# Performance work log

Measured on AMD Instinct MI355X. Metric: run time of the kernel, lower is better.

## Reference

```python
import jax, jax.numpy as jnp
import numpy as np

S, I, H, FC, O = 16384, 64, 1024, 128, 1


def setup_inputs() -> dict:
    key = jax.random.key(0)
    ks = jax.random.split(key, 9)
    s_lstm = 1.0 / np.sqrt(H)
    return {
        "input_seq": jax.random.normal(ks[0], (S, I), jnp.float32),
        "W_ih": jax.random.uniform(ks[1], (4 * H, I), jnp.float32, -s_lstm, s_lstm),
        "W_hh": jax.random.uniform(ks[2], (4 * H, H), jnp.float32, -s_lstm, s_lstm),
        "b_ih": jax.random.uniform(ks[3], (4 * H,), jnp.float32, -s_lstm, s_lstm),
        "b_hh": jax.random.uniform(ks[4], (4 * H,), jnp.float32, -s_lstm, s_lstm),
        "fc1_w": jax.random.uniform(ks[5], (FC, H), jnp.float32, -s_lstm, s_lstm),
        "fc1_b": jax.random.uniform(ks[6], (FC,), jnp.float32, -s_lstm, s_lstm),
        "fc2_w": jax.random.uniform(ks[7], (O, FC), jnp.float32, -1.0 / np.sqrt(FC), 1.0 / np.sqrt(FC)),
        "fc2_b": jax.random.uniform(ks[8], (O,), jnp.float32, -1.0 / np.sqrt(FC), 1.0 / np.sqrt(FC)),
    }


def _lstm_scan(x, W_ih, W_hh, b_ih, b_hh):
    # PyTorch gate order: i, f, g, o. batch=1 collapsed; x: [S, I]
    xg = x @ W_ih.T + (b_ih + b_hh)  # precompute input-side gates: [S, 4H]

    def step(carry, xg_t):
        h, c = carry
        gates = xg_t + h @ W_hh.T
        i, f, g, o = jnp.split(gates, 4)
        i = jax.nn.sigmoid(i)
        f = jax.nn.sigmoid(f)
        g = jnp.tanh(g)
        o = jax.nn.sigmoid(o)
        c = f * c + i * g
        h = o * jnp.tanh(c)
        return (h, c), h

    h0 = jnp.zeros((H,), x.dtype)
    c0 = jnp.zeros((H,), x.dtype)
    _, hs = jax.lax.scan(step, (h0, c0), xg)
    return hs  # [S, H]


def reference(input_seq, W_ih, W_hh, b_ih, b_hh, fc1_w, fc1_b, fc2_w, fc2_b):
    hs = _lstm_scan(input_seq, W_ih, W_hh, b_ih, b_hh)       # [S, H]
    x = jax.nn.relu(hs)                                       # relu on LSTM outputs
    x = jax.nn.relu(x @ fc1_w.T + fc1_b)                      # [S, 128]
    x = x @ fc2_w.T + fc2_b                                   # [S, 1]
    return x[-1]                                              # [1]
```

## Files before the change

### kernel.cpp

```cpp
#include <hip/hip_runtime.h>
#include <hip/hip_fp16.h>


#define S_LEN 16384
#define I_DIM 64
#define H_DIM 1024
#define NBLK  64
#define NTHR  1024

__device__ __forceinline__ float sigmoidf_(float x) { return 1.0f / (1.0f + __expf(-x)); }
__device__ __forceinline__ float tanh_fast(float x) { return 1.0f - 2.0f / (__expf(2.0f * x) + 1.0f); }

__device__ __forceinline__ unsigned pack_pair(unsigned tag, float h) {
    return (tag << 16) | (unsigned)__half_as_ushort(__float2half(h));
}
__device__ __forceinline__ float unpack_val(unsigned pk) {
    return __half2float(__ushort_as_half((unsigned short)(pk & 0xFFFFu)));
}

__global__ __launch_bounds__(NTHR, 4) void lstm_persistent(
    const float* __restrict__ xseq,
    const float* __restrict__ W_ih,
    const float* __restrict__ W_hh,
    const float* __restrict__ b_ih,
    const float* __restrict__ b_hh,
    unsigned* __restrict__ pairs)
{
    const int b   = blockIdx.x;
    const int tid = threadIdx.x;
    const int w   = tid >> 6;
    const int c   = tid & 63;
    const int g   = w >> 2;
    const int r0  = (w & 3) * 4;

    __shared__ float4 h_stage[H_DIM / 4];
    __shared__ float  x_stage[2][I_DIM];
    __shared__ float  gs[64];
    __shared__ float  bias_s[64];

    float4 wh[4][4];
    float  wi[4];
    #pragma unroll
    for (int q = 0; q < 4; ++q) {
        const int grow = g * H_DIM + 16 * b + r0 + q;
        const float4* wr = (const float4*)(W_hh + (size_t)grow * H_DIM);
        #pragma unroll
        for (int s = 0; s < 4; ++s) wh[q][s] = wr[s * 64 + c];
        wi[q] = W_ih[(size_t)grow * I_DIM + c];
    }
    if (tid < 64) {
        const int grow = (tid >> 4) * H_DIM + 16 * b + (tid & 15);
        bias_s[tid] = b_ih[grow] + b_hh[grow];
    }
    float cst = 0.0f;
    if (tid < H_DIM / 4) h_stage[tid] = make_float4(0.f, 0.f, 0.f, 0.f);
    if (tid < 16) ((float4*)x_stage[0])[tid] = ((const float4*)xseq)[tid];
    const bool own = (tid >> 4) == b;
    __syncthreads();

    for (int t = 0; t < S_LEN; ++t) {
        if (tid < 16 && t + 1 < S_LEN)
            ((float4*)x_stage[(t + 1) & 1])[tid] =
                ((const float4*)(xseq + (size_t)(t + 1) * I_DIM))[tid];

        float acc[4] = {0.f, 0.f, 0.f, 0.f};
        #pragma unroll
        for (int s = 0; s < 4; ++s) {
            const float4 hv = h_stage[s * 64 + c];
            #pragma unroll
            for (int q = 0; q < 4; ++q) {
                acc[q] = fmaf(wh[q][s].x, hv.x, acc[q]);
                acc[q] = fmaf(wh[q][s].y, hv.y, acc[q]);
                acc[q] = fmaf(wh[q][s].z, hv.z, acc[q]);
                acc[q] = fmaf(wh[q][s].w, hv.w, acc[q]);
            }
        }
        {
            const float xv = x_stage[t & 1][c];
            #pragma unroll
            for (int q = 0; q < 4; ++q) acc[q] = fmaf(wi[q], xv, acc[q]);
        }
        #pragma unroll
        for (int q = 0; q < 4; ++q) {
            #pragma unroll
            for (int off = 32; off > 0; off >>= 1)
                acc[q] += __shfl_xor(acc[q], off, 64);
        }
        if (c == 0) {
            #pragma unroll
            for (int q = 0; q < 4; ++q) gs[g * 16 + r0 + q] = acc[q];
        }
        __syncthreads();

        if (tid < 16) {
            const float pi  = gs[tid]      + bias_s[tid];
            const float pfg = gs[16 + tid] + bias_s[16 + tid];
            const float pg  = gs[32 + tid] + bias_s[32 + tid];
            const float po  = gs[48 + tid] + bias_s[48 + tid];
            const float ig = sigmoidf_(pi);
            const float fg = sigmoidf_(pfg);
            const float gg = tanh_fast(pg);
            const float og = sigmoidf_(po);
            cst = fg * cst + ig * gg;
            const float h = og * tanh_fast(cst);
            const unsigned pk = pack_pair((unsigned)(t + 1), h);
            __hip_atomic_store(&pairs[(size_t)(t & 1) * H_DIM + 16 * b + tid], pk,
                               __ATOMIC_RELAXED, __HIP_MEMORY_SCOPE_AGENT);
            ((float*)h_stage)[16 * b + tid] = unpack_val(pk);
        }

        if (t == S_LEN - 1) break;

        if (!own) {
            const unsigned tag = (unsigned)(t + 1);
            const unsigned* p = &pairs[(size_t)(t & 1) * H_DIM + tid];
            unsigned pk;
            for (;;) {
                pk = __hip_atomic_load(p, __ATOMIC_RELAXED, __HIP_MEMORY_SCOPE_AGENT);
                if ((pk >> 16) == tag) break;
                __builtin_amdgcn_s_sleep(1);
            }
            ((float*)h_stage)[tid] = unpack_val(pk);
        }
        __syncthreads();
    }
}

__global__ __launch_bounds__(256) void fc_head(
    const unsigned* __restrict__ pairs,
    const float* __restrict__ fc1_w,
    const float* __restrict__ fc1_b,
    const float* __restrict__ fc2_w,
    const float* __restrict__ fc2_b,
    float* __restrict__ out)
{
    const int tid = threadIdx.x;
    __shared__ float4 hr4[H_DIM / 4];
    __shared__ float  partial[256];
    __shared__ float  r1[128];

    const uint4 pa = ((const uint4*)(pairs + H_DIM))[tid];
    float4 hv = make_float4(__half2float(__ushort_as_half((unsigned short)(pa.x & 0xFFFFu))),
                            __half2float(__ushort_as_half((unsigned short)(pa.y & 0xFFFFu))),
                            __half2float(__ushort_as_half((unsigned short)(pa.z & 0xFFFFu))),
                            __half2float(__ushort_as_half((unsigned short)(pa.w & 0xFFFFu))));
    hv.x = fmaxf(hv.x, 0.f); hv.y = fmaxf(hv.y, 0.f);
    hv.z = fmaxf(hv.z, 0.f); hv.w = fmaxf(hv.w, 0.f);
    hr4[tid] = hv;
    __syncthreads();

    const int row = tid & 127, half = tid >> 7;
    const float4* wrow = (const float4*)(fc1_w + (size_t)row * H_DIM) + half * 128;
    float a0 = 0.f, a1 = 0.f;
    #pragma unroll 4
    for (int i = 0; i < 128; i += 2) {
        const float4 w0 = wrow[i],     h0 = hr4[half * 128 + i];
        const float4 w1 = wrow[i + 1], h1 = hr4[half * 128 + i + 1];
        a0 += w0.x * h0.x + w0.y * h0.y + w0.z * h0.z + w0.w * h0.w;
        a1 += w1.x * h1.x + w1.y * h1.y + w1.z * h1.z + w1.w * h1.w;
    }
    partial[tid] = a0 + a1;
    __syncthreads();
    if (tid < 128) {
        const float s = partial[tid] + partial[tid + 128] + fc1_b[tid];
        r1[tid] = fmaxf(s, 0.f);
    }
    __syncthreads();
    if (tid < 64) {
        float v = r1[tid] * fc2_w[tid] + r1[tid + 64] * fc2_w[tid + 64];
        #pragma unroll
        for (int off = 32; off > 0; off >>= 1) v += __shfl_xor(v, off, 64);
        if (tid == 0) out[0] = v + fc2_b[0];
    }
}

extern "C" void kernel_launch(void* const* d_in, const int* in_sizes, int n_in,
                              void* d_out, int out_size, void* d_ws, size_t ws_size,
                              hipStream_t stream) {
    (void)in_sizes; (void)n_in; (void)out_size; (void)ws_size;
    const float* xseq  = (const float*)d_in[0];
    const float* W_ih  = (const float*)d_in[1];
    const float* W_hh  = (const float*)d_in[2];
    const float* b_ih  = (const float*)d_in[3];
    const float* b_hh  = (const float*)d_in[4];
    const float* fc1_w = (const float*)d_in[5];
    const float* fc1_b = (const float*)d_in[6];
    const float* fc2_w = (const float*)d_in[7];
    const float* fc2_b = (const float*)d_in[8];
    unsigned* pairs = (unsigned*)d_ws;

    lstm_persistent<<<NBLK, NTHR, 0, stream>>>(xseq, W_ih, W_hh, b_ih, b_hh, pairs);
    fc_head<<<1, 256, 0, stream>>>(pairs, fc1_w, fc1_b, fc2_w, fc2_b, (float*)d_out);
}
```

Baseline: 39.72 ms.

## Poll hidden state with a single wavefront using 64-bit atomic loads

The cross-block handoff of the hidden state now uses one dedicated wavefront that polls all 1024 tagged entries with eight 64-bit atomic loads per lane, checking two tags per load, and writes the decoded values into shared memory. Previously about 1000 threads each spun on their own 32-bit entry with sleeps. The block's own slice is also read back from global memory rather than written locally, and the x prefetch moves to a separate wavefront. The goal is to cut polling traffic and wakeup latency on the serial critical path, at the cost of tight spinning without sleep and wavefront 15 doing every load.

Result: slower. 43.28 ms (+9.0%).

```diff
diff --git a/kernel.cpp b/kernel.cpp
--- a/kernel.cpp
+++ b/kernel.cpp
@@ -10,13 +10,6 @@
 
 __device__ __forceinline__ float sigmoidf_(float x) { return 1.0f / (1.0f + __expf(-x)); }
 __device__ __forceinline__ float tanh_fast(float x) { return 1.0f - 2.0f / (__expf(2.0f * x) + 1.0f); }
-
-__device__ __forceinline__ unsigned pack_pair(unsigned tag, float h) {
-    return (tag << 16) | (unsigned)__half_as_ushort(__float2half(h));
-}
-__device__ __forceinline__ float unpack_val(unsigned pk) {
-    return __half2float(__ushort_as_half((unsigned short)(pk & 0xFFFFu)));
-}
 
 __global__ __launch_bounds__(NTHR, 4) void lstm_persistent(
     const float* __restrict__ xseq,
@@ -55,13 +48,12 @@
     float cst = 0.0f;
     if (tid < H_DIM / 4) h_stage[tid] = make_float4(0.f, 0.f, 0.f, 0.f);
     if (tid < 16) ((float4*)x_stage[0])[tid] = ((const float4*)xseq)[tid];
-    const bool own = (tid >> 4) == b;
     __syncthreads();
 
     for (int t = 0; t < S_LEN; ++t) {
-        if (tid < 16 && t + 1 < S_LEN)
-            ((float4*)x_stage[(t + 1) & 1])[tid] =
-                ((const float4*)(xseq + (size_t)(t + 1) * I_DIM))[tid];
+        if (w == 14 && c < 16 && t + 1 < S_LEN)
+            ((float4*)x_stage[(t + 1) & 1])[c] =
+                ((const float4*)(xseq + (size_t)(t + 1) * I_DIM))[c];
 
         float acc[4] = {0.f, 0.f, 0.f, 0.f};
         #pragma unroll
@@ -103,24 +95,38 @@
             const float og = sigmoidf_(po);
             cst = fg * cst + ig * gg;
             const float h = og * tanh_fast(cst);
-            const unsigned pk = pack_pair((unsigned)(t + 1), h);
+            const unsigned pk = ((unsigned)(t + 1) << 16) |
+                                (unsigned)__half_as_ushort(__float2half(h));
             __hip_atomic_store(&pairs[(size_t)(t & 1) * H_DIM + 16 * b + tid], pk,
                                __ATOMIC_RELAXED, __HIP_MEMORY_SCOPE_AGENT);
-            ((float*)h_stage)[16 * b + tid] = unpack_val(pk);
         }
 
         if (t == S_LEN - 1) break;
 
-        if (!own) {
-            const unsigned tag = (unsigned)(t + 1);
-            const unsigned* p = &pairs[(size_t)(t & 1) * H_DIM + tid];
-            unsigned pk;
+        if (w == 15) {
+            const unsigned long long* P =
+                (const unsigned long long*)(pairs + (size_t)(t & 1) * H_DIM);
+            const unsigned long long tag = (unsigned long long)(unsigned)(t + 1);
+            const unsigned long long expv = (tag << 48) | (tag << 16);
+            const unsigned long long msk  = 0xFFFF0000FFFF0000ull;
+            unsigned long long v[8];
             for (;;) {
-                pk = __hip_atomic_load(p, __ATOMIC_RELAXED, __HIP_MEMORY_SCOPE_AGENT);
-                if ((pk >> 16) == tag) break;
-                __builtin_amdgcn_s_sleep(1);
+                bool ok = true;
+                #pragma unroll
+                for (int u = 0; u < 8; ++u) {
+                    v[u] = __hip_atomic_load(P + 64 * u + c,
+                                             __ATOMIC_RELAXED, __HIP_MEMORY_SCOPE_AGENT);
+                    ok = ok && ((v[u] & msk) == expv);
+                }
+                if (ok) break;
             }
-            ((float*)h_stage)[tid] = unpack_val(pk);
+            float2* hs2 = (float2*)h_stage;
+            #pragma unroll
+            for (int u = 0; u < 8; ++u) {
+                const float lo = __half2float(__ushort_as_half((unsigned short)(v[u] & 0xFFFFu)));
+                const float hi = __half2float(__ushort_as_half((unsigned short)((v[u] >> 32) & 0xFFFFu)));
+                hs2[64 * u + c] = make_float2(lo, hi);
+            }
         }
         __syncthreads();
     }
```
